# Kernel optimization log

Hardware: AMD Instinct MI355X
Metric: run time of the kernel (lower is better)

Reference implementation:

```python
import jax, jax.numpy as jnp
import numpy as np

B, S, H = 512, 100, 768
LAMB = 0.8

def setup_inputs() -> dict:
    key = jax.random.key(0)
    k1, k2, k3, k4 = jax.random.split(key, 4)
    scale = 1.0 / np.sqrt(H)
    return {
        "sent_vec": jax.random.normal(k1, (B, S, H), dtype=jnp.float32),
        "mask_cls": jnp.ones((B, S), dtype=jnp.int32),
        "W_cont": jax.random.normal(k2, (1, H), dtype=jnp.float32) * scale,
        "W_sim": jax.random.normal(k3, (H, H), dtype=jnp.float32) * scale,
        "W_rel": jax.random.normal(k4, (H, H), dtype=jnp.float32) * scale,
        "b_matrix": jnp.zeros((1, 1), dtype=jnp.float32),
    }

def reference(sent_vec, mask_cls, W_cont, W_sim, W_rel, b_matrix):
    # sent_vec: [B,S,H], mask_cls: [B,S] (all ones -> true_dim == S)
    m = mask_cls.astype(sent_vec.dtype)                       # [B,S]
    mask2 = m[:, :, None] * m[:, None, :]                     # mask_my_own [B,S,S]

    # Score_Cont[b,i,j] = W_cont . sent_vec[b,i]
    cont = jnp.einsum('h,bih->bi', W_cont[0], sent_vec)       # [B,S]
    # Score_Sim[b,i,j] = sent_i W_sim sent_j^T, masked
    sim = jnp.einsum('bih,hk,bjk->bij', sent_vec, W_sim, sent_vec) * mask2
    # Score_rel[b,i,j] = sent_i W_rel d_rep, masked
    d_rep = sent_vec.mean(axis=1)                             # [B,H]
    rel = jnp.einsum('bih,hk,bk->bi', sent_vec, W_rel, d_rep) # [B,S]

    q = jax.nn.sigmoid(rel[:, :, None] * mask2 + cont[:, :, None] + sim + b_matrix[0, 0])
    q = q * mask2                                             # [B,S,S]

    # D = diag(column sums of q); q @ D^{-1} divides columns by sum_vec
    sum_vec = q.sum(axis=1)                                   # [B,S]
    qD = q / sum_vec[:, None, :]                              # [B,S,S]

    I = jnp.eye(S, dtype=q.dtype)
    M = I[None, :, :] - LAMB * qD                             # [B,S,S]
    y = jnp.full((B, S, 1), 1.0 / S, dtype=q.dtype)
    # Final_score = (1-lamb) * inv(I - lamb q D^-1) @ y  (solve == inverse@mm)
    score = (1.0 - LAMB) * jnp.linalg.solve(M, y)[:, :, 0]    # [B,S]
    return score
```

## Files before the change

kernel.cpp:

```cpp
#include <hip/hip_runtime.h>
#include <math.h>

#define BB 512
#define SS 100
#define HH 768

typedef __bf16 bf16x8 __attribute__((ext_vector_type(8)));
typedef __bf16 bf16x4 __attribute__((ext_vector_type(4)));
typedef float f32x4 __attribute__((ext_vector_type(4)));
typedef float f32x16 __attribute__((ext_vector_type(16)));

__device__ __forceinline__ void gld16(const void* g, void* l) {
    __builtin_amdgcn_global_load_lds((const __attribute__((address_space(1))) char*)g,
                                     (__attribute__((address_space(3))) char*)l, 16, 0, 0);
}

__global__ __launch_bounds__(256) void k_drep(const float* __restrict__ X,
                                              float* __restrict__ drep) {
    int b = blockIdx.x, g = blockIdx.y;
    int lane = threadIdx.x & 63, w = threadIdx.x >> 6;
    const float4* xb = (const float4*)(X + (size_t)b * SS * HH);
    int c4 = g * 64 + lane;
    float4 s = {0.f, 0.f, 0.f, 0.f};
    for (int r = w; r < SS; r += 4) {
        float4 v = xb[r * 192 + c4];
        s.x += v.x; s.y += v.y; s.z += v.z; s.w += v.w;
    }
    __shared__ float4 red[4][64];
    red[w][lane] = s;
    __syncthreads();
    if (w == 0) {
        float4 a0 = red[0][lane], a1 = red[1][lane], a2 = red[2][lane], a3 = red[3][lane];
        float4 o;
        o.x = (a0.x + a1.x + a2.x + a3.x) * (1.0f / SS);
        o.y = (a0.y + a1.y + a2.y + a3.y) * (1.0f / SS);
        o.z = (a0.z + a1.z + a2.z + a3.z) * (1.0f / SS);
        o.w = (a0.w + a1.w + a2.w + a3.w) * (1.0f / SS);
        ((float4*)(drep + (size_t)b * HH))[c4] = o;
    }
}

__global__ __launch_bounds__(256) void k_gemm_nt(const float* __restrict__ A,
                                                 const float* __restrict__ Bm,
                                                 float* __restrict__ C,
                                                 int N, int K) {
    __shared__ float As[64 * 20];
    __shared__ float Bs[64 * 20];
    int tid = threadIdx.x;
    int ty = tid >> 4, tx = tid & 15;
    int m0 = blockIdx.y * 64, n0 = blockIdx.x * 64;
    int lr = tid >> 2, lc = (tid & 3) * 4;
    float acc[4][4] = {};
    for (int kt = 0; kt < K; kt += 16) {
        *(float4*)(As + lr * 20 + lc) = *(const float4*)(A + (size_t)(m0 + lr) * K + kt + lc);
        *(float4*)(Bs + lr * 20 + lc) = *(const float4*)(Bm + (size_t)(n0 + lr) * K + kt + lc);
        __syncthreads();
        #pragma unroll
        for (int k = 0; k < 16; k += 2) {
            float2 ar[4], br[4];
            #pragma unroll
            for (int ii = 0; ii < 4; ++ii) ar[ii] = *(const float2*)(As + (ty + 16 * ii) * 20 + k);
            #pragma unroll
            for (int jj = 0; jj < 4; ++jj) br[jj] = *(const float2*)(Bs + (tx + 16 * jj) * 20 + k);
            #pragma unroll
            for (int ii = 0; ii < 4; ++ii)
                #pragma unroll
                for (int jj = 0; jj < 4; ++jj)
                    acc[ii][jj] = fmaf(ar[ii].y, br[jj].y, fmaf(ar[ii].x, br[jj].x, acc[ii][jj]));
        }
        __syncthreads();
    }
    #pragma unroll
    for (int ii = 0; ii < 4; ++ii)
        #pragma unroll
        for (int jj = 0; jj < 4; ++jj)
            C[(size_t)(m0 + ty + 16 * ii) * N + n0 + tx + 16 * jj] = acc[ii][jj];
}

__global__ __launch_bounds__(256) void k_splitw(const float* __restrict__ W,
                                                __bf16* __restrict__ th,
                                                __bf16* __restrict__ tl) {
    __shared__ float tile[32][33];
    int bn = blockIdx.x * 32, bk = blockIdx.y * 32;
    int tx = threadIdx.x & 31, ty = threadIdx.x >> 5;
    for (int r = ty; r < 32; r += 8)
        tile[r][tx] = W[(size_t)(bk + r) * HH + bn + tx];
    __syncthreads();
    for (int r = ty; r < 32; r += 8) {
        float v = tile[tx][r];
        __bf16 hv = (__bf16)v;
        size_t idx = (size_t)(bn + r) * HH + bk + tx;
        th[idx] = hv;
        tl[idx] = (__bf16)(v - (float)hv);
    }
}

__global__ __launch_bounds__(512) void k_split_contrel(const float* __restrict__ X,
                                                       const float* __restrict__ Wc,
                                                       const float* __restrict__ tmat,
                                                       const float* __restrict__ bmat,
                                                       __bf16* __restrict__ Xh,
                                                       __bf16* __restrict__ Xl,
                                                       float* __restrict__ avec,
                                                       int b_off) {
    __shared__ float4 u4[192];
    int lb = blockIdx.x, half = blockIdx.y;
    int b = b_off + lb;
    int tid = threadIdx.x, lane = tid & 63, w = tid >> 6;
    for (int c = tid; c < 192; c += 512) {
        float4 wc = ((const float4*)Wc)[c];
        float4 tm = ((const float4*)(tmat + (size_t)b * HH))[c];
        float4 o = {wc.x + tm.x, wc.y + tm.y, wc.z + tm.z, wc.w + tm.w};
        u4[c] = o;
    }
    __syncthreads();
    float b00 = bmat[0];
    const float4* xb = (const float4*)(X + (size_t)b * SS * HH);
    bf16x4* xh4 = (bf16x4*)(Xh + (size_t)lb * SS * HH);
    bf16x4* xl4 = (bf16x4*)(Xl + (size_t)lb * SS * HH);
    int rend = half * 50 + 50;
    for (int r = half * 50 + w; r < rend; r += 8) {
        float s = 0.f;
        #pragma unroll
        for (int cc = 0; cc < 3; ++cc) {
            int c = cc * 64 + lane;
            float4 v = xb[r * 192 + c];
            float4 uu = u4[c];
            s = fmaf(v.x, uu.x, fmaf(v.y, uu.y, fmaf(v.z, uu.z, fmaf(v.w, uu.w, s))));
            bf16x4 hv, lv;
            hv[0] = (__bf16)v.x; lv[0] = (__bf16)(v.x - (float)hv[0]);
            hv[1] = (__bf16)v.y; lv[1] = (__bf16)(v.y - (float)hv[1]);
            hv[2] = (__bf16)v.z; lv[2] = (__bf16)(v.z - (float)hv[2]);
            hv[3] = (__bf16)v.w; lv[3] = (__bf16)(v.w - (float)hv[3]);
            xh4[r * 192 + c] = hv;
            xl4[r * 192 + c] = lv;
        }
        #pragma unroll
        for (int off = 32; off > 0; off >>= 1) s += __shfl_down(s, off);
        if (lane == 0) avec[(size_t)b * SS + r] = s + b00;
    }
}

__global__ __launch_bounds__(256) void k_gemm1_mfma(const __bf16* __restrict__ Ah_g,
                                                    const __bf16* __restrict__ Al_g,
                                                    const __bf16* __restrict__ Bh_g,
                                                    const __bf16* __restrict__ Bl_g,
                                                    __bf16* __restrict__ Yh,
                                                    __bf16* __restrict__ Yl) {
    __shared__ __align__(16) __bf16 lds[4 * 4096];
    __bf16* As_h = lds;
    __bf16* As_l = lds + 4096;
    __bf16* Bs_h = lds + 8192;
    __bf16* Bs_l = lds + 12288;
    const int tid = threadIdx.x;
    const int wave = tid >> 6, lane = tid & 63;
    const int wy = wave >> 1, wx = wave & 1;
    const size_t m0 = (size_t)blockIdx.y * 128;
    const int n0 = blockIdx.x * 128;

    const size_t gra0 = m0 + lane;
    const size_t gra1 = m0 + 64 + lane;
    const size_t grb0 = n0 + lane;
    const size_t grb1 = n0 + 64 + lane;
    const int lds_base = wave * 1024;

    const int arow = wy * 64 + (lane & 31);
    const int brow = wx * 64 + (lane & 31);
    const int loct = lane >> 5;

    f32x16 acc[2][2] = {};
    for (int kt = 0; kt < HH; kt += 32) {
        const int gcol = kt + wave * 8;
        gld16(Ah_g + gra0 * HH + gcol, As_h + lds_base);
        gld16(Ah_g + gra1 * HH + gcol, As_h + lds_base + 512);
        gld16(Al_g + gra0 * HH + gcol, As_l + lds_base);
        gld16(Al_g + gra1 * HH + gcol, As_l + lds_base + 512);
        gld16(Bh_g + grb0 * HH + gcol, Bs_h + lds_base);
        gld16(Bh_g + grb1 * HH + gcol, Bs_h + lds_base + 512);
        gld16(Bl_g + grb0 * HH + gcol, Bs_l + lds_base);
        gld16(Bl_g + grb1 * HH + gcol, Bs_l + lds_base + 512);
        __syncthreads();
        #pragma unroll
        for (int kh = 0; kh < 2; ++kh) {
            const int ob = (kh * 2 + loct) * 1024;
            bf16x8 fah[2], fal[2], fbh[2], fbl[2];
            #pragma unroll
            for (int t = 0; t < 2; ++t) {
                fah[t] = *(const bf16x8*)(As_h + ob + (arow + t * 32) * 8);
                fal[t] = *(const bf16x8*)(As_l + ob + (arow + t * 32) * 8);
                fbh[t] = *(const bf16x8*)(Bs_h + ob + (brow + t * 32) * 8);
                fbl[t] = *(const bf16x8*)(Bs_l + ob + (brow + t * 32) * 8);
            }
            #pragma unroll
            for (int ti = 0; ti < 2; ++ti)
                #pragma unroll
                for (int tj = 0; tj < 2; ++tj) {
                    acc[ti][tj] = __builtin_amdgcn_mfma_f32_32x32x16_bf16(fal[ti], fbh[tj], acc[ti][tj], 0, 0, 0);
                    acc[ti][tj] = __builtin_amdgcn_mfma_f32_32x32x16_bf16(fah[ti], fbl[tj], acc[ti][tj], 0, 0, 0);
                    acc[ti][tj] = __builtin_amdgcn_mfma_f32_32x32x16_bf16(fah[ti], fbh[tj], acc[ti][tj], 0, 0, 0);
                }
        }
        __syncthreads();
    }
    const int rbase = 4 * (lane >> 5);
    const int colb = lane & 31;
    #pragma unroll
    for (int ti = 0; ti < 2; ++ti) {
        #pragma unroll
        for (int tj = 0; tj < 2; ++tj) {
            int col = n0 + wx * 64 + tj * 32 + colb;
            #pragma unroll
            for (int r = 0; r < 16; ++r) {
                int row = wy * 64 + ti * 32 + (r & 3) + 8 * (r >> 2) + rbase;
                float v = acc[ti][tj][r];
                __bf16 hv = (__bf16)v;
                size_t idx = (m0 + row) * HH + col;
                Yh[idx] = hv;
                Yl[idx] = (__bf16)(v - (float)hv);
            }
        }
    }
}

__global__ __launch_bounds__(256) void k_gemm2_mfma(const __bf16* __restrict__ Yh,
                                                    const __bf16* __restrict__ Yl,
                                                    const __bf16* __restrict__ Xh,
                                                    const __bf16* __restrict__ Xl,
                                                    const float* __restrict__ avec,
                                                    float* __restrict__ q, int b_off) {
    __shared__ __align__(16) __bf16 lds[4 * 4096];
    __shared__ float av_s[SS];
    __bf16* As_h = lds;
    __bf16* As_l = lds + 4096;
    __bf16* Bs_h = lds + 8192;
    __bf16* Bs_l = lds + 12288;
    const int bl = blockIdx.x;
    const int b = b_off + bl;
    const __bf16* Ah_g = Yh + (size_t)bl * SS * HH;
    const __bf16* Al_g = Yl + (size_t)bl * SS * HH;
    const __bf16* Bh_g = Xh + (size_t)bl * SS * HH;
    const __bf16* Bl_g = Xl + (size_t)bl * SS * HH;
    const int tid = threadIdx.x;
    const int wave = tid >> 6, lane = tid & 63;
    const int wy = wave >> 1, wx = wave & 1;
    if (tid < SS) av_s[tid] = avec[(size_t)b * SS + tid];

    const size_t r0 = lane;
    const size_t r1 = (64 + lane) < SS ? (64 + lane) : SS - 1;
    const int lds_base = wave * 1024;

    const int arow = wy * 64 + (lane & 31);
    const int brow = wx * 64 + (lane & 31);
    const int loct = lane >> 5;

    f32x16 acc[2][2] = {};
    for (int kt = 0; kt < HH; kt += 32) {
        const int gcol = kt + wave * 8;
        gld16(Ah_g + r0 * HH + gcol, As_h + lds_base);
        gld16(Ah_g + r1 * HH + gcol, As_h + lds_base + 512);
        gld16(Al_g + r0 * HH + gcol, As_l + lds_base);
        gld16(Al_g + r1 * HH + gcol, As_l + lds_base + 512);
        gld16(Bh_g + r0 * HH + gcol, Bs_h + lds_base);
        gld16(Bh_g + r1 * HH + gcol, Bs_h + lds_base + 512);
        gld16(Bl_g + r0 * HH + gcol, Bs_l + lds_base);
        gld16(Bl_g + r1 * HH + gcol, Bs_l + lds_base + 512);
        __syncthreads();
        #pragma unroll
        for (int kh = 0; kh < 2; ++kh) {
            const int ob = (kh * 2 + loct) * 1024;
            bf16x8 fah[2], fal[2], fbh[2], fbl[2];
            #pragma unroll
            for (int t = 0; t < 2; ++t) {
                fah[t] = *(const bf16x8*)(As_h + ob + (arow + t * 32) * 8);
                fal[t] = *(const bf16x8*)(As_l + ob + (arow + t * 32) * 8);
                fbh[t] = *(const bf16x8*)(Bs_h + ob + (brow + t * 32) * 8);
                fbl[t] = *(const bf16x8*)(Bs_l + ob + (brow + t * 32) * 8);
            }
            #pragma unroll
            for (int ti = 0; ti < 2; ++ti)
                #pragma unroll
                for (int tj = 0; tj < 2; ++tj) {
                    acc[ti][tj] = __builtin_amdgcn_mfma_f32_32x32x16_bf16(fal[ti], fbh[tj], acc[ti][tj], 0, 0, 0);
                    acc[ti][tj] = __builtin_amdgcn_mfma_f32_32x32x16_bf16(fah[ti], fbl[tj], acc[ti][tj], 0, 0, 0);
                    acc[ti][tj] = __builtin_amdgcn_mfma_f32_32x32x16_bf16(fah[ti], fbh[tj], acc[ti][tj], 0, 0, 0);
                }
        }
        __syncthreads();
    }
    float* qb = q + (size_t)b * SS * SS;
    const int rbase = 4 * (lane >> 5);
    const int colb = lane & 31;
    #pragma unroll
    for (int ti = 0; ti < 2; ++ti) {
        #pragma unroll
        for (int tj = 0; tj < 2; ++tj) {
            int j = wx * 64 + tj * 32 + colb;
            if (j >= SS) continue;
            #pragma unroll
            for (int r = 0; r < 16; ++r) {
                int i = wy * 64 + ti * 32 + (r & 3) + 8 * (r >> 2) + rbase;
                if (i >= SS) continue;
                float v = acc[ti][tj][r] + av_s[i];
                qb[(size_t)i * SS + j] = 1.0f / (1.0f + __expf(-v));
            }
        }
    }
}

__global__ __launch_bounds__(128) void k_solve(const float* __restrict__ q,
                                               float* __restrict__ out) {
    __shared__ __align__(16) float m[SS * SS];
    __shared__ __align__(16) float csinv[SS];
    __shared__ __align__(16) float x0[SS], x1[SS];
    int b = blockIdx.x, tid = threadIdx.x;
    const float* qb = q + (size_t)b * SS * SS;
    for (int e4 = tid; e4 < SS * SS / 4; e4 += 128)
        *(float4*)(m + e4 * 4) = *(const float4*)(qb + (size_t)e4 * 4);
    __syncthreads();
    if (tid < SS) {
        float s = 0.f;
        for (int i = 0; i < SS; ++i) s += m[i * SS + tid];
        csinv[tid] = 0.8f / s;
        x0[tid] = 1.0f / SS;
    }
    __syncthreads();
    float4 mreg[25];
    if (tid < SS) {
        #pragma unroll
        for (int j4 = 0; j4 < 25; ++j4) {
            float4 mv = *(const float4*)(m + tid * SS + j4 * 4);
            float4 cv = *(const float4*)(csinv + j4 * 4);
            mreg[j4].x = mv.x * cv.x;
            mreg[j4].y = mv.y * cv.y;
            mreg[j4].z = mv.z * cv.z;
            mreg[j4].w = mv.w * cv.w;
        }
    } else {
        #pragma unroll
        for (int j4 = 0; j4 < 25; ++j4) mreg[j4] = float4{0, 0, 0, 0};
    }
    __syncthreads();
    #pragma unroll 1
    for (int it = 0; it < 56; ++it) {
        const float* xr = (it & 1) ? x1 : x0;
        float* xw = (it & 1) ? x0 : x1;
        if (tid < SS) {
            float sx = 0.f, sy = 0.f, sz = 0.f, sw = 0.f;
            #pragma unroll
            for (int j4 = 0; j4 < 25; ++j4) {
                float4 xv = *(const float4*)(xr + j4 * 4);
                sx = fmaf(mreg[j4].x, xv.x, sx);
                sy = fmaf(mreg[j4].y, xv.y, sy);
                sz = fmaf(mreg[j4].z, xv.z, sz);
                sw = fmaf(mreg[j4].w, xv.w, sw);
            }
            xw[tid] = 0.002f + ((sx + sy) + (sz + sw));
        }
        __syncthreads();
    }
    if (tid < SS) out[(size_t)b * SS + tid] = x0[tid];
}

extern "C" void kernel_launch(void* const* d_in, const int* in_sizes, int n_in,
                              void* d_out, int out_size, void* d_ws, size_t ws_size,
                              hipStream_t stream) {
    (void)in_sizes; (void)n_in; (void)out_size;
    const float* X    = (const float*)d_in[0];
    const float* Wc   = (const float*)d_in[2];
    const float* Wsim = (const float*)d_in[3];
    const float* Wrel = (const float*)d_in[4];
    const float* bmat = (const float*)d_in[5];
    float* out = (float*)d_out;

    char* ws = (char*)d_ws;
    size_t off = 0;
    float*  qbuf = (float*)(ws + off);  off += (size_t)BB * SS * SS * 4;
    float*  drep = (float*)(ws + off);  off += (size_t)BB * HH * 4;
    float*  tmat = (float*)(ws + off);  off += (size_t)BB * HH * 4;
    float*  avec = (float*)(ws + off);  off += (size_t)BB * SS * 4;
    __bf16* Wth  = (__bf16*)(ws + off); off += (size_t)HH * HH * 2;
    __bf16* Wtl  = (__bf16*)(ws + off); off += (size_t)HH * HH * 2;

    int CB = 512;
    while (CB > 128 && off + 4 * (size_t)CB * SS * HH * 2 > ws_size) CB >>= 1;
    size_t xsz = (size_t)CB * SS * HH * 2;
    __bf16* Xh = (__bf16*)(ws + off); off += xsz;
    __bf16* Xl = (__bf16*)(ws + off); off += xsz;
    __bf16* Yh = (__bf16*)(ws + off); off += xsz;
    __bf16* Yl = (__bf16*)(ws + off); off += xsz;

    k_drep<<<dim3(BB, 3), 256, 0, stream>>>(X, drep);
    k_gemm_nt<<<dim3(HH / 64, BB / 64), 256, 0, stream>>>(drep, Wrel, tmat, HH, HH);
    k_splitw<<<dim3(HH / 32, HH / 32), 256, 0, stream>>>(Wsim, Wth, Wtl);

    for (int c = 0; c < BB; c += CB) {
        k_split_contrel<<<dim3(CB, 2), 512, 0, stream>>>(X + (size_t)c * SS * HH, Wc, tmat, bmat, Xh, Xl, avec, c);
        k_gemm1_mfma<<<dim3(HH / 128, CB * SS / 128), 256, 0, stream>>>(Xh, Xl, Wth, Wtl, Yh, Yl);
        k_gemm2_mfma<<<CB, 256, 0, stream>>>(Yh, Yl, Xh, Xl, avec, qbuf, c);
    }
    k_solve<<<BB, 128, 0, stream>>>(qbuf, out);
}
```

Measured before the change: 828.9 us.

## Register-prefetch next K tile in split-bf16 GEMMs instead of direct global-to-LDS loads

Both split-precision MFMA GEMM kernels stop using direct global-to-LDS loads. They now load the next K tile into registers while computing on the current LDS tile, then store to LDS at the top of the next iteration. The per-thread load mapping also changes: each lane reads a contiguous 16-byte chunk across four lanes per row, which gives more coalesced global reads than the earlier one-row-per-lane pattern. The aim is to hide global latency behind the MFMA work, at the cost of more registers, explicit LDS stores, and a wasted wrap-around prefetch on the last iteration.

```diff
diff --git a/kernel.cpp b/kernel.cpp
--- a/kernel.cpp
+++ b/kernel.cpp
@@ -9,11 +9,6 @@
 typedef __bf16 bf16x4 __attribute__((ext_vector_type(4)));
 typedef float f32x4 __attribute__((ext_vector_type(4)));
 typedef float f32x16 __attribute__((ext_vector_type(16)));
-
-__device__ __forceinline__ void gld16(const void* g, void* l) {
-    __builtin_amdgcn_global_load_lds((const __attribute__((address_space(1))) char*)g,
-                                     (__attribute__((address_space(3))) char*)l, 16, 0, 0);
-}
 
 __global__ __launch_bounds__(256) void k_drep(const float* __restrict__ X,
                                               float* __restrict__ drep) {
@@ -158,38 +153,51 @@
     const size_t m0 = (size_t)blockIdx.y * 128;
     const int n0 = blockIdx.x * 128;
 
-    const size_t gra0 = m0 + lane;
-    const size_t gra1 = m0 + 64 + lane;
-    const size_t grb0 = n0 + lane;
-    const size_t grb1 = n0 + 64 + lane;
-    const int lds_base = wave * 1024;
+    const int sr0 = wave * 32 + (lane >> 2);
+    const int sr1 = sr0 + 16;
+    const int sc  = lane & 3;
+    const int wsl0 = sc * 1024 + sr0 * 8;
+    const int wsl1 = sc * 1024 + sr1 * 8;
+    const size_t ga0 = (m0 + sr0) * HH + sc * 8;
+    const size_t ga1 = (m0 + sr1) * HH + sc * 8;
+    const size_t gb0 = (size_t)(n0 + sr0) * HH + sc * 8;
+    const size_t gb1 = (size_t)(n0 + sr1) * HH + sc * 8;
 
     const int arow = wy * 64 + (lane & 31);
     const int brow = wx * 64 + (lane & 31);
     const int loct = lane >> 5;
 
     f32x16 acc[2][2] = {};
+    bf16x8 pah0, pah1, pal0, pal1, pbh0, pbh1, pbl0, pbl1;
+    pah0 = *(const bf16x8*)(Ah_g + ga0); pah1 = *(const bf16x8*)(Ah_g + ga1);
+    pal0 = *(const bf16x8*)(Al_g + ga0); pal1 = *(const bf16x8*)(Al_g + ga1);
+    pbh0 = *(const bf16x8*)(Bh_g + gb0); pbh1 = *(const bf16x8*)(Bh_g + gb1);
+    pbl0 = *(const bf16x8*)(Bl_g + gb0); pbl1 = *(const bf16x8*)(Bl_g + gb1);
+
     for (int kt = 0; kt < HH; kt += 32) {
-        const int gcol = kt + wave * 8;
-        gld16(Ah_g + gra0 * HH + gcol, As_h + lds_base);
-        gld16(Ah_g + gra1 * HH + gcol, As_h + lds_base + 512);
-        gld16(Al_g + gra0 * HH + gcol, As_l + lds_base);
-        gld16(Al_g + gra1 * HH + gcol, As_l + lds_base + 512);
-        gld16(Bh_g + grb0 * HH + gcol, Bs_h + lds_base);
-        gld16(Bh_g + grb1 * HH + gcol, Bs_h + lds_base + 512);
-        gld16(Bl_g + grb0 * HH + gcol, Bs_l + lds_base);
-        gld16(Bl_g + grb1 * HH + gcol, Bs_l + lds_base + 512);
-        __syncthreads();
+        __syncthreads();
+        *(bf16x8*)(As_h + wsl0) = pah0; *(bf16x8*)(As_h + wsl1) = pah1;
+        *(bf16x8*)(As_l + wsl0) = pal0; *(bf16x8*)(As_l + wsl1) = pal1;
+        *(bf16x8*)(Bs_h + wsl0) = pbh0; *(bf16x8*)(Bs_h + wsl1) = pbh1;
+        *(bf16x8*)(Bs_l + wsl0) = pbl0; *(bf16x8*)(Bs_l + wsl1) = pbl1;
+        __syncthreads();
+        int ktn = kt + 32; if (ktn >= HH) ktn = 0;
+        pah0 = *(const bf16x8*)(Ah_g + ga0 + ktn); pah1 = *(const bf16x8*)(Ah_g + ga1 + ktn);
+        pal0 = *(const bf16x8*)(Al_g + ga0 + ktn); pal1 = *(const bf16x8*)(Al_g + ga1 + ktn);
+        pbh0 = *(const bf16x8*)(Bh_g + gb0 + ktn); pbh1 = *(const bf16x8*)(Bh_g + gb1 + ktn);
+        pbl0 = *(const bf16x8*)(Bl_g + gb0 + ktn); pbl1 = *(const bf16x8*)(Bl_g + gb1 + ktn);
         #pragma unroll
         for (int kh = 0; kh < 2; ++kh) {
             const int ob = (kh * 2 + loct) * 1024;
             bf16x8 fah[2], fal[2], fbh[2], fbl[2];
             #pragma unroll
             for (int t = 0; t < 2; ++t) {
-                fah[t] = *(const bf16x8*)(As_h + ob + (arow + t * 32) * 8);
-                fal[t] = *(const bf16x8*)(As_l + ob + (arow + t * 32) * 8);
-                fbh[t] = *(const bf16x8*)(Bs_h + ob + (brow + t * 32) * 8);
-                fbl[t] = *(const bf16x8*)(Bs_l + ob + (brow + t * 32) * 8);
+                const int oa = ob + (arow + t * 32) * 8;
+                const int obb = ob + (brow + t * 32) * 8;
+                fah[t] = *(const bf16x8*)(As_h + oa);
+                fal[t] = *(const bf16x8*)(As_l + oa);
+                fbh[t] = *(const bf16x8*)(Bs_h + obb);
+                fbl[t] = *(const bf16x8*)(Bs_l + obb);
             }
             #pragma unroll
             for (int ti = 0; ti < 2; ++ti)
@@ -200,7 +208,6 @@
                     acc[ti][tj] = __builtin_amdgcn_mfma_f32_32x32x16_bf16(fah[ti], fbh[tj], acc[ti][tj], 0, 0, 0);
                 }
         }
-        __syncthreads();
     }
     const int rbase = 4 * (lane >> 5);
     const int colb = lane & 31;
@@ -245,36 +252,51 @@
     const int wy = wave >> 1, wx = wave & 1;
     if (tid < SS) av_s[tid] = avec[(size_t)b * SS + tid];
 
-    const size_t r0 = lane;
-    const size_t r1 = (64 + lane) < SS ? (64 + lane) : SS - 1;
-    const int lds_base = wave * 1024;
+    const int sr0 = wave * 32 + (lane >> 2);
+    const int sr1 = sr0 + 16;
+    const int sc  = lane & 3;
+    const int wsl0 = sc * 1024 + sr0 * 8;
+    const int wsl1 = sc * 1024 + sr1 * 8;
+    const int r0c = sr0 < SS ? sr0 : SS - 1;
+    const int r1c = sr1 < SS ? sr1 : SS - 1;
+    const size_t ga0 = (size_t)r0c * HH + sc * 8;
+    const size_t ga1 = (size_t)r1c * HH + sc * 8;
 
     const int arow = wy * 64 + (lane & 31);
     const int brow = wx * 64 + (lane & 31);
     const int loct = lane >> 5;
 
     f32x16 acc[2][2] = {};
+    bf16x8 pah0, pah1, pal0, pal1, pbh0, pbh1, pbl0, pbl1;
+    pah0 = *(const bf16x8*)(Ah_g + ga0); pah1 = *(const bf16x8*)(Ah_g + ga1);
+    pal0 = *(const bf16x8*)(Al_g + ga0); pal1 = *(const bf16x8*)(Al_g + ga1);
+    pbh0 = *(const bf16x8*)(Bh_g + ga0); pbh1 = *(const bf16x8*)(Bh_g + ga1);
+    pbl0 = *(const bf16x8*)(Bl_g + ga0); pbl1 = *(const bf16x8*)(Bl_g + ga1);
+
     for (int kt = 0; kt < HH; kt += 32) {
-        const int gcol = kt + wave * 8;
-        gld16(Ah_g + r0 * HH + gcol, As_h + lds_base);
-        gld16(Ah_g + r1 * HH + gcol, As_h + lds_base + 512);
-        gld16(Al_g + r0 * HH + gcol, As_l + lds_base);
-        gld16(Al_g + r1 * HH + gcol, As_l + lds_base + 512);
-        gld16(Bh_g + r0 * HH + gcol, Bs_h + lds_base);
-        gld16(Bh_g + r1 * HH + gcol, Bs_h + lds_base + 512);
-        gld16(Bl_g + r0 * HH + gcol, Bs_l + lds_base);
-        gld16(Bl_g + r1 * HH + gcol, Bs_l + lds_base + 512);
-        __syncthreads();
+        __syncthreads();
+        *(bf16x8*)(As_h + wsl0) = pah0; *(bf16x8*)(As_h + wsl1) = pah1;
+        *(bf16x8*)(As_l + wsl0) = pal0; *(bf16x8*)(As_l + wsl1) = pal1;
+        *(bf16x8*)(Bs_h + wsl0) = pbh0; *(bf16x8*)(Bs_h + wsl1) = pbh1;
+        *(bf16x8*)(Bs_l + wsl0) = pbl0; *(bf16x8*)(Bs_l + wsl1) = pbl1;
+        __syncthreads();
+        int ktn = kt + 32; if (ktn >= HH) ktn = 0;
+        pah0 = *(const bf16x8*)(Ah_g + ga0 + ktn); pah1 = *(const bf16x8*)(Ah_g + ga1 + ktn);
+        pal0 = *(const bf16x8*)(Al_g + ga0 + ktn); pal1 = *(const bf16x8*)(Al_g + ga1 + ktn);
+        pbh0 = *(const bf16x8*)(Bh_g + ga0 + ktn); pbh1 = *(const bf16x8*)(Bh_g + ga1 + ktn);
+        pbl0 = *(const bf16x8*)(Bl_g + ga0 + ktn); pbl1 = *(const bf16x8*)(Bl_g + ga1 + ktn);
         #pragma unroll
         for (int kh = 0; kh < 2; ++kh) {
             const int ob = (kh * 2 + loct) * 1024;
             bf16x8 fah[2], fal[2], fbh[2], fbl[2];
             #pragma unroll
             for (int t = 0; t < 2; ++t) {
-                fah[t] = *(const bf16x8*)(As_h + ob + (arow + t * 32) * 8);
-                fal[t] = *(const bf16x8*)(As_l + ob + (arow + t * 32) * 8);
-                fbh[t] = *(const bf16x8*)(Bs_h + ob + (brow + t * 32) * 8);
-                fbl[t] = *(const bf16x8*)(Bs_l + ob + (brow + t * 32) * 8);
+                const int oa = ob + (arow + t * 32) * 8;
+                const int obb = ob + (brow + t * 32) * 8;
+                fah[t] = *(const bf16x8*)(As_h + oa);
+                fal[t] = *(const bf16x8*)(As_l + oa);
+                fbh[t] = *(const bf16x8*)(Bs_h + obb);
+                fbl[t] = *(const bf16x8*)(Bs_l + obb);
             }
             #pragma unroll
             for (int ti = 0; ti < 2; ++ti)
@@ -285,7 +307,6 @@
                     acc[ti][tj] = __builtin_amdgcn_mfma_f32_32x32x16_bf16(fah[ti], fbh[tj], acc[ti][tj], 0, 0, 0);
                 }
         }
-        __syncthreads();
     }
     float* qb = q + (size_t)b * SS * SS;
     const int rbase = 4 * (lane >> 5);
```

Result: faster. 753.4 us (-9.1%).
